# Kernel optimization log

Measured on AMD Instinct MI355X. Metric: run time of the kernel, lower is better.

The kernel has to match this reference:

```python
import jax, jax.numpy as jnp
import numpy as np

NUM_HEADS = 7


def setup_inputs() -> dict:
    key = jax.random.key(0)
    k1, k2 = jax.random.split(key)
    x = jax.random.normal(k1, (1024, 896, 7, 7), dtype=jnp.float32)
    W_qkv = jax.random.normal(k2, (2688, 896), dtype=jnp.float32) * 0.02
    return {"x": x, "W_qkv": W_qkv}


def reference(x, W_qkv):
    B, C, H, W = x.shape
    N = H * W  # 49 tokens
    head_dim = C // NUM_HEADS
    scale = head_dim ** -0.5

    # tokens: [B, N, C]
    tokens = x.reshape(B, C, N).transpose(0, 2, 1)
    # qkv: [B, N, 3C] -> [3, B, heads, N, head_dim]
    qkv = jnp.einsum('bnc,dc->bnd', tokens, W_qkv)
    qkv = qkv.reshape(B, N, 3, NUM_HEADS, head_dim).transpose(2, 0, 3, 1, 4)
    q, k = qkv[0] * scale, qkv[1]
    # attn: [B, heads, N, N] (attn_drop rate 0 -> identity; proj output discarded by module)
    attn = jax.nn.softmax(jnp.einsum('bhnd,bhmd->bhnm', q, k), axis=-1)

    # min over heads -> fused attention [B, N, N]
    fused = attn.min(axis=1)
    flat = fused.reshape(B, N * N)

    k_top = int(N * N * 0.9)  # 2160
    _, indices = jax.lax.top_k(-flat, k_top)  # [B, k_top]
    # replicate torch bug: indices flattened across batch, zeros removed,
    # then only flat[0] is masked.
    idx = indices.reshape(-1)
    zero_mask = jnp.zeros(N * N, dtype=bool).at[idx].set(idx != 0)
    flat = flat.at[0].set(jnp.where(zero_mask, 0.0, flat[0]))
    fused = flat.reshape(B, N, N)

    # rollout normalization: (A + I)/2, divide by row-sum WITHOUT keepdim
    # (torch broadcasting divides column j by row-sum of row j)
    a = (fused + jnp.eye(N, dtype=fused.dtype)) * 0.5
    s = a.sum(axis=-1)  # [B, N]
    final_result = a / s[:, None, :]  # matmul with identity == itself

    att = final_result.mean(axis=1).reshape(B, 1, H, W)
    rx = x * att + x
    return rx
```

## Files before the change

### kernel.cpp

```cpp
#include <hip/hip_runtime.h>
#include <hip/hip_bf16.h>
#include <hip/hip_fp8.h>

#define B_    1024
#define C_    896
#define N_    49
#define NN    2401
#define HD    128
#define NH    7
#define CQK   1792
#define KTOP  2160
#define SCALE 0.08838834764831845f

typedef unsigned short ushort_t;
typedef unsigned char u8;
typedef unsigned int u32;
typedef short bf16x8 __attribute__((ext_vector_type(8)));
typedef float f32x4  __attribute__((ext_vector_type(4)));

__device__ __forceinline__ u8 f2fp8(float f) {
  __hip_fp8_e4m3 q(f);
  return (u8)q.__x;
}

__device__ __forceinline__ void gload16(const void* g, void* l) {
  __builtin_amdgcn_global_load_lds((const __attribute__((address_space(1))) u32*)g,
                                   (__attribute__((address_space(3))) u32*)l, 16, 0, 0);
}

__global__ void k_convW(const float* __restrict__ W, u8* __restrict__ Wf8) {
  int i = blockIdx.x * 256 + threadIdx.x;
  if (i >= CQK * C_ / 4) return;
  const float* wp = W + (size_t)i * 4;
  u32 r = (u32)f2fp8(wp[0]) | ((u32)f2fp8(wp[1]) << 8)
        | ((u32)f2fp8(wp[2]) << 16) | ((u32)f2fp8(wp[3]) << 24);
  ((u32*)Wf8)[i] = r;
}

__global__ __launch_bounds__(256) void k_tr(const float* __restrict__ x,
                                            u8* __restrict__ tokens,
                                            int boff) {
  __shared__ u8 T2[49][80];
  const int bid = blockIdx.x;
  const int bl  = bid / 14;
  const int cg  = bid % 14;
  const float* xb = x + (size_t)(boff + bl) * (C_ * N_) + (size_t)cg * 64 * N_;
  for (int idx = threadIdx.x; idx < 784; idx += 256) {
    float4 f = ((const float4*)xb)[idx];
    int e0 = idx * 4;
#pragma unroll
    for (int u = 0; u < 4; ++u) {
      int e = e0 + u;
      int ci = e / 49, n = e - ci * 49;
      float v = (u == 0) ? f.x : (u == 1) ? f.y : (u == 2) ? f.z : f.w;
      T2[n][ci] = f2fp8(v);
    }
  }
  __syncthreads();
  u8* tb = tokens + (size_t)(bl * 49) * C_ + cg * 64;
  for (int idx = threadIdx.x; idx < 49 * 4; idx += 256) {
    int n = idx >> 2, c16 = (idx & 3) * 16;
    *(uint4*)(tb + (size_t)n * C_ + c16) = *(const uint4*)&T2[n][c16];
  }
}

#define GEMM_LDS 131072

__global__ __launch_bounds__(512, 2) void k_gemm(const u8* __restrict__ tokens,
                                                 const u8* __restrict__ Wf8,
                                                 u8* __restrict__ QK,
                                                 int MG) {
  extern __shared__ u8 gsm[];
  u8* sA = gsm;
  u8* sB = gsm + 65536;

  const int nwg = gridDim.x;
  const int q8 = nwg >> 3, r8 = nwg & 7;
  const int xcd = blockIdx.x & 7, idx8 = blockIdx.x >> 3;
  const int tile = (xcd < r8 ? xcd * (q8 + 1) : r8 * (q8 + 1) + (xcd - r8) * q8) + idx8;

  const int mt = tile / 7, nt = tile - mt * 7;
  const int m0 = mt * 256, n0 = nt * 256;

  const int t = threadIdx.x;
  const int w = t >> 6, l = t & 63;
  const int lrow = l & 15, hi = l >> 4;
  const int wm = w & 1, wn = w >> 1;

  const int srow8 = t >> 3;
  const int sp16  = ((t & 7) ^ (srow8 & 7)) * 16;
  const u8* aSrc[4];
  const u8* bSrc[4];
#pragma unroll
  for (int u = 0; u < 4; ++u) {
    int ar = m0 + u * 64 + srow8; if (ar >= MG) ar = MG - 1;
    aSrc[u] = tokens + (size_t)ar * C_ + sp16;
    bSrc[u] = Wf8 + (size_t)(n0 + u * 64 + srow8) * C_ + sp16;
  }
  u8* ldsA = sA + t * 16;
  u8* ldsB = sB + t * 16;

  const int key = lrow & 7;
  int pOff[4];
#pragma unroll
  for (int c = 0; c < 4; ++c)
    pOff[c] = ((2 * c + (hi >> 1)) ^ key) * 16 + (hi & 1) * 8;
  const int aRow0 = (wm * 128 + lrow) * 128;
  const int bRow0 = (wn * 64 + lrow) * 128;

  f32x4 acc[8][4];
#pragma unroll
  for (int m = 0; m < 8; ++m)
#pragma unroll
    for (int n = 0; n < 4; ++n) acc[m][n] = (f32x4){0.f, 0.f, 0.f, 0.f};

  auto STAGE = [&](int kt) {
    const int so = (kt & 1) * 32768;
    const int kc = kt * 128;
#pragma unroll
    for (int u = 0; u < 4; ++u) {
      gload16(aSrc[u] + kc, ldsA + so + u * 8192);
      gload16(bSrc[u] + kc, ldsB + so + u * 8192);
    }
  };

  STAGE(0);
  __syncthreads();

#pragma unroll 1
  for (int kt = 0; kt < 7; ++kt) {
    const int so = (kt & 1) * 32768;
    if (kt < 6) STAGE(kt + 1);
#pragma unroll
    for (int c = 0; c < 4; ++c) {
      long a[8], bv[4];
#pragma unroll
      for (int m = 0; m < 8; ++m)
        a[m] = *(const long*)(sA + so + aRow0 + m * 2048 + pOff[c]);
#pragma unroll
      for (int n = 0; n < 4; ++n)
        bv[n] = *(const long*)(sB + so + bRow0 + n * 2048 + pOff[c]);
      __builtin_amdgcn_s_setprio(1);
#pragma unroll
      for (int m = 0; m < 8; ++m)
#pragma unroll
        for (int n = 0; n < 4; ++n)
          acc[m][n] = __builtin_amdgcn_mfma_f32_16x16x32_fp8_fp8(a[m], bv[n], acc[m][n], 0, 0, 0);
      __builtin_amdgcn_s_setprio(0);
    }
    __syncthreads();
  }

#pragma unroll
  for (int m = 0; m < 8; ++m) {
#pragma unroll
    for (int n = 0; n < 4; ++n) {
      int gcol = n0 + wn * 64 + n * 16 + lrow;
      float sc = (gcol < C_) ? SCALE : 1.0f;
#pragma unroll
      for (int r = 0; r < 4; ++r) {
        int grow = m0 + wm * 128 + m * 16 + hi * 4 + r;
        if (grow < MG)
          QK[(size_t)grow * CQK + gcol] = f2fp8(acc[m][n][r] * sc);
      }
    }
  }
}

__global__ __launch_bounds__(256) void k_attn2(const u8* __restrict__ QK,
                                               float* __restrict__ att,
                                               u32* __restrict__ gmask,
                                               float* __restrict__ fused0,
                                               int boff) {
  __shared__ u32 lmask[76];
  const int tid  = threadIdx.x;
  const int wid  = tid >> 6;
  const int lane = tid & 63;
  const int lrow = lane & 15;
  const int hi   = lane >> 4;
  const int lk   = hi * 8;
  const int bloc = blockIdx.x * 4 + wid;
  const int bg   = boff + bloc;
  const f32x4 z4 = {0.f, 0.f, 0.f, 0.f};

  for (int p = tid; p < 76; p += 256) lmask[p] = 0u;
  __syncthreads();

  const u8* Qb = QK + (size_t)bloc * 49 * CQK;
  const u8* Kb = Qb + C_;

  int rr[4];
#pragma unroll
  for (int i = 0; i < 4; ++i) {
    int r = i * 16 + lrow; if (r > 48) r = 48;
    rr[i] = r;
  }

  float fu[4][16];

  for (int h = 0; h < NH; ++h) {
    f32x4 acc[4][4];
#pragma unroll
    for (int qt = 0; qt < 4; ++qt)
#pragma unroll
      for (int kt = 0; kt < 4; ++kt) acc[qt][kt] = z4;

#pragma unroll
    for (int e = 0; e < 4; ++e) {
      long kf[4], qf[4];
#pragma unroll
      for (int kt = 0; kt < 4; ++kt)
        kf[kt] = *(const long*)(Kb + (size_t)rr[kt] * CQK + h * HD + e * 32 + lk);
#pragma unroll
      for (int qt = 0; qt < 4; ++qt)
        qf[qt] = *(const long*)(Qb + (size_t)rr[qt] * CQK + h * HD + e * 32 + lk);
#pragma unroll
      for (int qt = 0; qt < 4; ++qt)
#pragma unroll
        for (int kt = 0; kt < 4; ++kt)
          acc[qt][kt] = __builtin_amdgcn_mfma_f32_16x16x32_fp8_fp8(kf[kt], qf[qt],
                                                                   acc[qt][kt], 0, 0, 0);
    }

#pragma unroll
    for (int qt = 0; qt < 4; ++qt) {
      float mx = -1e30f;
#pragma unroll
      for (int kt = 0; kt < 4; ++kt)
#pragma unroll
        for (int r = 0; r < 4; ++r) {
          int k = kt * 16 + hi * 4 + r;
          if (k < N_) mx = fmaxf(mx, acc[qt][kt][r]);
        }
      mx = fmaxf(mx, __shfl_xor(mx, 16));
      mx = fmaxf(mx, __shfl_xor(mx, 32));
      float ev[16];
      float sum = 0.f;
#pragma unroll
      for (int kt = 0; kt < 4; ++kt)
#pragma unroll
        for (int r = 0; r < 4; ++r) {
          int k = kt * 16 + hi * 4 + r;
          float e = (k < N_) ? __expf(acc[qt][kt][r] - mx) : 0.f;
          ev[kt * 4 + r] = e;
          sum += e;
        }
      sum += __shfl_xor(sum, 16);
      sum += __shfl_xor(sum, 32);
      float rs = 1.0f / sum;
#pragma unroll
      for (int i = 0; i < 16; ++i) {
        float p = ev[i] * rs;
        fu[qt][i] = (h == 0) ? p : fminf(fu[qt][i], p);
      }
    }
  }

  u32 vb[4][16];
#pragma unroll
  for (int qt = 0; qt < 4; ++qt) {
    int q = qt * 16 + lrow;
#pragma unroll
    for (int i = 0; i < 16; ++i) {
      int k = (i >> 2) * 16 + hi * 4 + (i & 3);
      vb[qt][i] = (q < N_ && k < N_) ? __builtin_bit_cast(u32, fu[qt][i]) : 0x7F800000u;
    }
  }

  u32 thr = 0;
  for (int bit = 29; bit >= 0; --bit) {
    u32 cand = thr | (1u << bit);
    int c = 0;
#pragma unroll
    for (int qt = 0; qt < 4; ++qt)
#pragma unroll
      for (int i = 0; i < 16; ++i) c += (vb[qt][i] < cand) ? 1 : 0;
    c += __shfl_xor(c, 1);  c += __shfl_xor(c, 2);  c += __shfl_xor(c, 4);
    c += __shfl_xor(c, 8);  c += __shfl_xor(c, 16); c += __shfl_xor(c, 32);
    if (c < KTOP) thr = cand;
  }

#pragma unroll
  for (int qt = 0; qt < 4; ++qt) {
    int q = qt * 16 + lrow;
#pragma unroll
    for (int i = 0; i < 16; ++i) {
      int k = (i >> 2) * 16 + hi * 4 + (i & 3);
      int p = q * N_ + k;
      if (q < N_ && k < N_ && p != 0 && vb[qt][i] <= thr)
        atomicOr(&lmask[p >> 5], 1u << (p & 31));
    }
  }

  float rsv[4];
#pragma unroll
  for (int qt = 0; qt < 4; ++qt) {
    int q = qt * 16 + lrow;
    float s = 0.f;
#pragma unroll
    for (int i = 0; i < 16; ++i) {
      int k = (i >> 2) * 16 + hi * 4 + (i & 3);
      s += (q < N_ && k < N_) ? fu[qt][i] : 0.f;
    }
    s += __shfl_xor(s, 16); s += __shfl_xor(s, 32);
    rsv[qt] = s;
  }
  float csv[16];
#pragma unroll
  for (int i = 0; i < 16; ++i) {
    int k = (i >> 2) * 16 + hi * 4 + (i & 3);
    float s = 0.f;
#pragma unroll
    for (int qt = 0; qt < 4; ++qt) {
      int q = qt * 16 + lrow;
      s += (q < N_ && k < N_) ? fu[qt][i] : 0.f;
    }
    s += __shfl_xor(s, 1); s += __shfl_xor(s, 2);
    s += __shfl_xor(s, 4); s += __shfl_xor(s, 8);
    csv[i] = s;
  }
#pragma unroll
  for (int kt = 0; kt < 4; ++kt)
#pragma unroll
    for (int r = 0; r < 4; ++r) {
      int tt = kt * 16 + hi * 4 + r;
      float rv = __shfl(rsv[kt], hi * 4 + r);
      if (lrow == 0 && tt < N_)
        att[(size_t)bg * N_ + tt] = (csv[kt * 4 + r] + 1.0f) / (49.0f * (rv + 1.0f));
    }

  if (bg == 0) {
#pragma unroll
    for (int qt = 0; qt < 4; ++qt) {
      int q = qt * 16 + lrow;
#pragma unroll
      for (int i = 0; i < 16; ++i) {
        int k = (i >> 2) * 16 + hi * 4 + (i & 3);
        if (q < N_ && k < N_) fused0[q * N_ + k] = fu[qt][i];
      }
    }
  }

  __syncthreads();
  for (int p = tid; p < 76; p += 256)
    if (lmask[p]) atomicOr(&gmask[p], lmask[p]);
}

__global__ void k_fix0(const float* __restrict__ fused0, const u32* __restrict__ gmask,
                       float* __restrict__ att) {
  __shared__ float fl[NN];
  const int t = threadIdx.x;
  for (int p = t; p < NN; p += 256) {
    float vv = fused0[p];
    if ((gmask[p >> 5] >> (p & 31)) & 1u) vv = 0.f;
    fl[p] = vv;
  }
  __syncthreads();
  if (t < N_) {
    float rs = 0.f, cs = 0.f;
    for (int m = 0; m < N_; ++m) { rs += fl[t * N_ + m]; cs += fl[m * N_ + t]; }
    att[t] = (cs + 1.0f) / (49.0f * (rs + 1.0f));
  }
}

__global__ void k_rx(const float* __restrict__ x, const float* __restrict__ att,
                     float* __restrict__ out) {
  const int total4 = B_ * C_ * N_ / 4;
  for (int g = blockIdx.x * 256 + threadIdx.x; g < total4; g += gridDim.x * 256) {
    u32 e0 = (u32)g * 4u;
    u32 b = e0 / (u32)(C_ * N_);
    u32 r = e0 - b * (u32)(C_ * N_);
    u32 n = r % (u32)N_;
    const float4 xv = ((const float4*)x)[g];
    const float* ab = att + b * N_;
    float a0 = ab[n];
    u32 n1 = n + 1;  if (n1 == N_) n1 = 0;  float a1 = ab[n1];
    u32 n2 = n1 + 1; if (n2 == N_) n2 = 0;  float a2 = ab[n2];
    u32 n3 = n2 + 1; if (n3 == N_) n3 = 0;  float a3 = ab[n3];
    float4 o;
    o.x = xv.x * (1.f + a0); o.y = xv.y * (1.f + a1);
    o.z = xv.z * (1.f + a2); o.w = xv.w * (1.f + a3);
    ((float4*)out)[g] = o;
  }
}

extern "C" void kernel_launch(void* const* d_in, const int* in_sizes, int n_in,
                              void* d_out, int out_size, void* d_ws, size_t ws_size,
                              hipStream_t stream) {
  const float* x = (const float*)d_in[0];
  const float* W = (const float*)d_in[1];
  float* out = (float*)d_out;
  char* ws = (char*)d_ws;

  const size_t fixed = 200704  + 1605632  + 1024  + 9632 ;
  int G = 256;
  const int cands[3] = {1024, 512, 256};
  for (int i = 0; i < 3; ++i) {
    if (fixed + (size_t)cands[i] * 49 * CQK <= ws_size) { G = cands[i]; break; }
  }

  const size_t qkbytes = (size_t)G * 49 * CQK;
  u8*       QKg    = (u8*)ws;
  float*    att    = (float*)(ws + qkbytes);
  u8*       Wf8    = (u8*)(ws + qkbytes + 200704);
  u32*      gmask  = (u32*)(ws + qkbytes + 200704 + 1605632);
  float*    fused0 = (float*)(ws + qkbytes + 200704 + 1605632 + 1024);
  u8*       tokens = (u8*)d_out;

  hipMemsetAsync(gmask, 0, 76 * sizeof(u32), stream);
  k_convW<<<(CQK * C_ / 4 + 255) / 256, 256, 0, stream>>>(W, Wf8);

  hipFuncSetAttribute((const void*)k_gemm, hipFuncAttributeMaxDynamicSharedMemorySize, GEMM_LDS);

  const int ngroups = B_ / G;
  for (int g = 0; g < ngroups; ++g) {
    const int boff = g * G;
    const int MG = G * 49;
    const int mtc = MG / 256;
    k_tr<<<G * 14, 256, 0, stream>>>(x, tokens, boff);
    k_gemm<<<mtc * 7, 512, GEMM_LDS, stream>>>(tokens, Wf8, QKg, MG);
    k_attn2<<<G / 4, 256, 0, stream>>>(QKg, att, gmask, fused0, boff);
  }

  k_fix0<<<1, 256, 0, stream>>>(fused0, gmask, att);
  k_rx<<<4096, 256, 0, stream>>>(x, att, out);
}
```

Measured before the change: 332.9 us.

## Use MI355 scaled 16x16x128 FP8 MFMA for QK projection GEMM

Replaces the four 16x16x32 fp8 MFMAs per k-chunk with a single gfx950 mfma_scale_f32_16x16x128_f8f6f4 instruction using unit scales (0x7F exponent). Each lane now loads 32 contiguous bytes per row through two 16-byte swizzled LDS reads, and A fragments are loaded in two halves to limit register pressure. The intent is to raise matrix-core throughput and cut the instruction count for the dominant projection GEMM. The risk is that the k-element ordering within each lane must match between A and B, and that the larger operand vectors may increase register use.

```diff
diff --git a/kernel.cpp b/kernel.cpp
--- a/kernel.cpp
+++ b/kernel.cpp
@@ -15,8 +15,11 @@
 typedef unsigned short ushort_t;
 typedef unsigned char u8;
 typedef unsigned int u32;
-typedef short bf16x8 __attribute__((ext_vector_type(8)));
 typedef float f32x4  __attribute__((ext_vector_type(4)));
+typedef int   i32x4  __attribute__((ext_vector_type(4)));
+typedef int   i32x8  __attribute__((ext_vector_type(8)));
+
+#define SCALE1 0x7F7F7F7F
 
 __device__ __forceinline__ u8 f2fp8(float f) {
   __hip_fp8_e4m3 q(f);
@@ -101,10 +104,7 @@
   u8* ldsB = sB + t * 16;
 
   const int key = lrow & 7;
-  int pOff[4];
-#pragma unroll
-  for (int c = 0; c < 4; ++c)
-    pOff[c] = ((2 * c + (hi >> 1)) ^ key) * 16 + (hi & 1) * 8;
+  const int p0 = ((2 * hi) ^ key) * 16;
   const int aRow0 = (wm * 128 + lrow) * 128;
   const int bRow0 = (wn * 64 + lrow) * 128;
 
@@ -122,6 +122,11 @@
       gload16(aSrc[u] + kc, ldsA + so + u * 8192);
       gload16(bSrc[u] + kc, ldsB + so + u * 8192);
     }
+  };
+  auto LD32 = [&](const u8* base) -> i32x8 {
+    i32x4 lo = *(const i32x4*)(base + p0);
+    i32x4 hv = *(const i32x4*)(base + (p0 ^ 16));
+    return __builtin_shufflevector(lo, hv, 0, 1, 2, 3, 4, 5, 6, 7);
   };
 
   STAGE(0);
@@ -131,21 +136,25 @@
   for (int kt = 0; kt < 7; ++kt) {
     const int so = (kt & 1) * 32768;
     if (kt < 6) STAGE(kt + 1);
-#pragma unroll
-    for (int c = 0; c < 4; ++c) {
-      long a[8], bv[4];
-#pragma unroll
-      for (int m = 0; m < 8; ++m)
-        a[m] = *(const long*)(sA + so + aRow0 + m * 2048 + pOff[c]);
-#pragma unroll
-      for (int n = 0; n < 4; ++n)
-        bv[n] = *(const long*)(sB + so + bRow0 + n * 2048 + pOff[c]);
+    i32x8 b8[4];
+#pragma unroll
+    for (int n = 0; n < 4; ++n)
+      b8[n] = LD32(sB + so + bRow0 + n * 2048);
+#pragma unroll
+    for (int mh = 0; mh < 2; ++mh) {
+      i32x8 av[4];
+#pragma unroll
+      for (int mm = 0; mm < 4; ++mm)
+        av[mm] = LD32(sA + so + aRow0 + (mh * 4 + mm) * 2048);
       __builtin_amdgcn_s_setprio(1);
 #pragma unroll
-      for (int m = 0; m < 8; ++m)
+      for (int mm = 0; mm < 4; ++mm)
 #pragma unroll
         for (int n = 0; n < 4; ++n)
-          acc[m][n] = __builtin_amdgcn_mfma_f32_16x16x32_fp8_fp8(a[m], bv[n], acc[m][n], 0, 0, 0);
+          acc[mh * 4 + mm][n] = __builtin_amdgcn_mfma_scale_f32_16x16x128_f8f6f4(
+              av[mm], b8[n], acc[mh * 4 + mm][n],
+              0 , 0 ,
+              0, SCALE1, 0, SCALE1);
       __builtin_amdgcn_s_setprio(0);
     }
     __syncthreads();
```

Result: faster. 292.0 us (-12.3%).
